# Optimization experiments

Measured on AMD Instinct MI355X. Metric: run time of the kernel, lower is better.

Reference implementation:

```python
import jax, jax.numpy as jnp
import numpy as np

B, T, V, K = 4, 1024, 32000, 50000
EPS_T, EPS_M = 1e-8, 1e-12


def setup_inputs() -> dict:
    key = jax.random.key(0)
    k1, k2, k3, k4 = jax.random.split(key, 4)
    probs = jax.random.uniform(k1, (B, T, V), dtype=jnp.float32)
    # normalize so rows are valid distributions (faithful to softmax outputs)
    probs = probs / probs.sum(-1, keepdims=True)
    target_probs = jax.random.uniform(k2, (K,), dtype=jnp.float32) * (1.0 / K)
    target_oov = jax.random.uniform(k3, (1,), dtype=jnp.float32)
    mask = jnp.ones((B, T), dtype=bool)
    pairs = jax.random.randint(k4, (K, 2), 0, V, dtype=jnp.int64 if jax.config.jax_enable_x64 else jnp.int32)
    return {"probs": probs, "target_probs": target_probs, "target_oov": target_oov,
            "mask": mask, "pairs": pairs}


def reference(probs, target_probs, target_oov, mask, pairs):
    a = pairs[:, 0]  # (K,)
    b = pairs[:, 1]
    p_t = probs[:, :-1, :]   # (B, T-1, V)
    p_t1 = probs[:, 1:, :]
    pair_mask = (mask[:, :-1] & mask[:, 1:]).astype(jnp.float32)  # (B, T-1)
    # gather bigram probs: (B, T-1, K) joint, masked sum over batch/seq
    joint = p_t[..., a] * p_t1[..., b]
    topk_sum = jnp.einsum('btk,bt->k', joint, pair_mask)  # (K,)
    n_pairs = pair_mask.sum()

    # finalize
    n = jnp.maximum(n_pairs, 1.0)
    model_top = jnp.maximum(topk_sum / n, EPS_M)
    model_oov = jnp.clip(1.0 - model_top.sum(), EPS_M, 1.0 - EPS_T)
    tgt = jnp.maximum(target_probs, EPS_T)
    t_oov = jnp.maximum(target_oov[0], EPS_T)
    kl_top = (model_top * (jnp.log(model_top) - jnp.log(tgt))).sum()
    kl_oov = model_oov * (jnp.log(model_oov) - jnp.log(t_oov))
    return kl_top + kl_oov
```

## Files before the change

kernel.cpp:

```cpp
#include <hip/hip_runtime.h>
#include <stdint.h>

#define B_   4
#define T_   1024
#define V_   32000
#define K_   50000
#define N_   (B_*(T_-1))
#define TPB  1024
#define U_   49
#define KP   (TPB*U_)
#define POS_PER_BLK 16
#define G1   ((N_ + POS_PER_BLK - 1)/POS_PER_BLK)
#define EPSTGT 1e-8f
#define EPSMOD 1e-12f
#define W4   (V_/4)
#define NGRP (KP/64)
#define SCAP (2*NGRP)
#define PINV 0xFFFFFFFFu

__device__ __forceinline__ uint32_t bf16rne(float x) {
    uint32_t u = __float_as_uint(x);
    u += 0x7FFFu + ((u >> 16) & 1u);
    return u >> 16;
}
__device__ __forceinline__ uint2 pack4(float4 v) {
    uint2 pk;
    pk.x = bf16rne(v.x) | (bf16rne(v.y) << 16);
    pk.y = bf16rne(v.z) | (bf16rne(v.w) << 16);
    return pk;
}
__device__ __forceinline__ void stage_row(const float* __restrict__ probs, int r,
                                          ushort* dst, int tid) {
    const float4* src = (const float4*)(probs + (size_t)r * V_);
    for (int i = tid; i < W4; i += TPB) {
        *(uint2*)(dst + i * 4) = pack4(src[i]);
    }
}

#define GATHER(pkv, accv) do {                                          \
    uint32_t ao_ = (pkv) >> 16, bo_ = (pkv) & 0xFFFFu;                  \
    ushort av_ = *(const ushort*)(rp + ao_);                            \
    ushort bv_ = *(const ushort*)(rq + bo_);                            \
    accv = fmaf(__uint_as_float((uint32_t)av_ << 16),                   \
                __uint_as_float((uint32_t)bv_ << 16), accv);            \
} while (0)

__global__ __launch_bounds__(1024) void k_perm(const int* __restrict__ pairs,
                                               uint32_t* __restrict__ ppk,
                                               uint32_t* __restrict__ perm,
                                               uint32_t* __restrict__ ovf,
                                               uint32_t* __restrict__ holes) {
    __shared__ uint32_t hist[32][32];
    __shared__ uint32_t boff[32][32];
    __shared__ uint32_t cnt[32][32];
    __shared__ uint32_t binc[32], rot[32];
    __shared__ uint32_t novf, nhole;
    const int tid = threadIdx.x;

    ((uint32_t*)hist)[tid] = 0;
    if (tid == 0) { novf = 0; nhole = 0; }
    __syncthreads();

    for (int k = tid; k < K_; k += 1024) {
        uint32_t a = (uint32_t)pairs[2 * k];
        uint32_t b = (uint32_t)pairs[2 * k + 1];
        atomicAdd(&hist[(a >> 1) & 31][(b >> 1) & 31], 1u);
    }
    __syncthreads();

    if (tid < 32) {
        uint32_t s = 0;
        for (int j = 0; j < 32; ++j) { boff[tid][j] = s; s += hist[tid][j]; }
        binc[tid] = s;
        rot[tid] = ((uint32_t)tid * s) >> 5;
    }
    __syncthreads();
    ((uint32_t*)cnt)[tid] = 0;
    for (int s = tid; s < KP; s += 1024) { ppk[s] = 0; perm[s] = PINV; }
    __syncthreads();

    for (int k = tid; k < K_; k += 1024) {
        uint32_t a = (uint32_t)pairs[2 * k];
        uint32_t b = (uint32_t)pairs[2 * k + 1];
        uint32_t aw = (a >> 1) & 31, bw = (b >> 1) & 31;
        uint32_t j = boff[aw][bw] + atomicAdd(&cnt[aw][bw], 1u);
        uint32_t c = binc[aw];
        uint32_t jp = j + rot[aw]; if (jp >= c) jp -= c;
        uint32_t pk = ((a * 2u) << 16) | (b * 2u);
        if (jp < SCAP) {
            uint32_t s = ((jp >> 1) << 6) + aw + ((jp & 1u) << 5);
            ppk[s] = pk; perm[s] = (uint32_t)k;
        } else {
            uint32_t i = atomicAdd(&novf, 1u);
            ovf[2 * i] = pk; ovf[2 * i + 1] = (uint32_t)k;
        }
    }
    __syncthreads();

    for (int s = tid; s < KP; s += 1024) {
        if (perm[s] == PINV) { uint32_t i = atomicAdd(&nhole, 1u); holes[i] = (uint32_t)s; }
    }
    __syncthreads();
    for (uint32_t i = tid; i < novf; i += 1024) {
        uint32_t s = holes[i];
        ppk[s] = ovf[2 * i]; perm[s] = ovf[2 * i + 1];
    }
}

__global__ void k_mask(const unsigned char* __restrict__ mask, float* __restrict__ scalars) {
    __shared__ int red[16];
    int tid = threadIdx.x;
    int cnt = 0;
    for (int n = tid; n < N_; n += 1024) {
        int b = n / (T_ - 1);
        int t = n - b * (T_ - 1);
        int r = b * T_ + t;
        cnt += (mask[r] && mask[r + 1]) ? 1 : 0;
    }
    for (int off = 32; off > 0; off >>= 1) cnt += __shfl_down(cnt, off, 64);
    int wid = tid >> 6, lid = tid & 63;
    if (lid == 0) red[wid] = cnt;
    __syncthreads();
    if (tid == 0) {
        int s = 0;
        for (int w = 0; w < 16; ++w) s += red[w];
        scalars[0] = (float)s;
    }
}

__global__ __launch_bounds__(TPB) void k_main(
    const float* __restrict__ probs,
    const unsigned char* __restrict__ mask,
    const uint32_t* __restrict__ ppk,
    float* __restrict__ partials, int S, int direct)
{
    __shared__ __align__(16) ushort rows[2][V_];
    __shared__ unsigned char mask_s[32];
    const int tid = threadIdx.x;
    const int g = blockIdx.x;
    const int n0 = g * POS_PER_BLK;
    const int n1 = min(N_, n0 + POS_PER_BLK);

    int r0 = n0 + n0 / (T_ - 1);
    int r1 = r0 + 1;
    const int rbase = r0;
    {
        int rlast = (n1 - 1) + (n1 - 1) / (T_ - 1) + 1;
        int nrows = rlast - rbase + 1;
        if (tid < nrows) mask_s[tid] = mask[rbase + tid];
    }

    float acc[U_];
#pragma unroll
    for (int u = 0; u < U_; ++u) acc[u] = 0.f;

    stage_row(probs, r0, rows[r0 & 1], tid);
    stage_row(probs, r1, rows[r1 & 1], tid);

    const uint32_t* pp = ppk + tid;

    for (int n = n0; n < n1; ++n) {
        const int nn = n + 1;
        const bool more = (nn < n1);
        const int nr0 = nn + nn / (T_ - 1);
        const int nr1 = nr0 + 1;
        const int pre_row = more ? ((nr0 == r1) ? nr1 : nr0) : -1;
        const bool extra = more && (nr0 != r1);
        const int ld_row = (pre_row >= 0) ? pre_row : 0;
        const float4* src = (const float4*)(probs + (size_t)ld_row * V_);

        __syncthreads();

        uint32_t pkA[28];
#pragma unroll
        for (int j = 0; j < 28; ++j) pkA[j] = pp[j * TPB];
        __builtin_amdgcn_sched_barrier(0);
        float4 L0[4];
#pragma unroll
        for (int j = 0; j < 4; ++j) L0[j] = src[tid + j * TPB];
        __builtin_amdgcn_sched_barrier(0);

        const bool active = mask_s[r0 - rbase] && mask_s[r1 - rbase];
        const char* rp = (const char*)rows[r0 & 1];
        const char* rq = (const char*)rows[r1 & 1];

        if (active) {
#pragma unroll
            for (int j = 0; j < 14; ++j) GATHER(pkA[j], acc[j]);
        }
        uint32_t pkB[21];
#pragma unroll
        for (int j = 0; j < 21; ++j) pkB[j] = pp[(28 + j) * TPB];
        __builtin_amdgcn_sched_barrier(0);
        if (active) {
#pragma unroll
            for (int j = 14; j < 28; ++j) GATHER(pkA[j], acc[j]);
        }
        uint2 P0[4];
#pragma unroll
        for (int j = 0; j < 4; ++j) P0[j] = pack4(L0[j]);
        float4 L1[4];
#pragma unroll
        for (int j = 0; j < 4; ++j) {
            int i = tid + (4 + j) * TPB;
            L1[j] = src[(i < W4) ? i : 0];
        }
        __builtin_amdgcn_sched_barrier(0);
        if (active) {
#pragma unroll
            for (int j = 0; j < 21; ++j) GATHER(pkB[j], acc[28 + j]);
        }

        __syncthreads();

        if (pre_row >= 0) {
            ushort* dst = rows[pre_row & 1];
#pragma unroll
            for (int j = 0; j < 4; ++j)
                *(uint2*)(dst + (tid + j * TPB) * 4) = P0[j];
#pragma unroll
            for (int j = 0; j < 4; ++j) {
                int i = tid + (4 + j) * TPB;
                if (i < W4) *(uint2*)(dst + i * 4) = pack4(L1[j]);
            }
            if (extra) stage_row(probs, nr1, rows[nr1 & 1], tid);
        }
        r0 = nr0; r1 = nr1;
    }

    if (direct) {
        float* slot = partials + (size_t)g * KP;
#pragma unroll
        for (int u = 0; u < U_; ++u) slot[u * TPB + tid] = acc[u];
    } else {
        float* slot = partials + (size_t)(g % S) * KP;
#pragma unroll
        for (int u = 0; u < U_; ++u) atomicAdd(slot + u * TPB + tid, acc[u]);
    }
}

__global__ void k_reduce(const float* __restrict__ partials, const uint32_t* __restrict__ perm,
                         const float* __restrict__ tgt,
                         float* __restrict__ scalars, int S) {
    int si = blockIdx.x * 256 + threadIdx.x;
    float n = fmaxf(scalars[0], 1.0f);
    float mt = 0.f, term = 0.f;
    if (si < KP) {
        uint32_t k = perm[si];
        if (k != PINV) {
            float ts = 0.f;
            for (int s = 0; s < S; ++s) ts += partials[(size_t)s * KP + si];
            mt = fmaxf(ts / n, EPSMOD);
            float tg = fmaxf(tgt[k], EPSTGT);
            term = mt * (__logf(mt) - __logf(tg));
        }
    }
    for (int off = 32; off > 0; off >>= 1) {
        mt += __shfl_down(mt, off, 64);
        term += __shfl_down(term, off, 64);
    }
    __shared__ float rm[4], rt[4];
    int wid = threadIdx.x >> 6, lid = threadIdx.x & 63;
    if (lid == 0) { rm[wid] = mt; rt[wid] = term; }
    __syncthreads();
    if (threadIdx.x == 0) {
        float sm = 0.f, st = 0.f;
        for (int w = 0; w < 4; ++w) { sm += rm[w]; st += rt[w]; }
        atomicAdd(&scalars[1], sm);
        atomicAdd(&scalars[2], st);
    }
}

__global__ void k_final(const float* __restrict__ scalars, const float* __restrict__ toov,
                        float* __restrict__ out) {
    float S1 = scalars[1], S2 = scalars[2];
    float moov = 1.f - S1;
    moov = fminf(fmaxf(moov, EPSMOD), 1.f - EPSTGT);
    float tv = fmaxf(toov[0], EPSTGT);
    out[0] = S2 + moov * (__logf(moov) - __logf(tv));
}

extern "C" void kernel_launch(void* const* d_in, const int* in_sizes, int n_in,
                              void* d_out, int out_size, void* d_ws, size_t ws_size,
                              hipStream_t stream) {
    const float* probs = (const float*)d_in[0];
    const float* tgt   = (const float*)d_in[1];
    const float* toov  = (const float*)d_in[2];
    const unsigned char* mask = (const unsigned char*)d_in[3];
    const int* pairs   = (const int*)d_in[4];
    float* out = (float*)d_out;

    char* ws = (char*)d_ws;
    uint32_t* ppk   = (uint32_t*)(ws + 0);
    uint32_t* perm  = (uint32_t*)(ws + 200704);
    uint32_t* ovf   = (uint32_t*)(ws + 401408);
    uint32_t* holes = (uint32_t*)(ws + 801536);
    size_t off_sc = 1002240;
    float* scalars = (float*)(ws + off_sc);
    size_t off_pt = off_sc + 256;
    float* partials = (float*)(ws + off_pt);

    long avail = (long)ws_size - (long)off_pt;
    int smax = (int)(avail / ((long)KP * 4));
    int direct = (smax >= G1) ? 1 : 0;
    int S = direct ? G1 : (smax < 1 ? 1 : (smax > 64 ? 64 : smax));

    hipMemsetAsync(ws + off_sc, 0, 256, stream);
    if (!direct) hipMemsetAsync(partials, 0, (size_t)S * KP * 4, stream);
    k_perm<<<1, 1024, 0, stream>>>(pairs, ppk, perm, ovf, holes);
    k_mask<<<1, 1024, 0, stream>>>(mask, scalars);
    k_main<<<G1, TPB, 0, stream>>>(probs, mask, ppk, partials, S, direct);
    k_reduce<<<(KP + 255) / 256, 256, 0, stream>>>(partials, perm, tgt, scalars, S);
    k_final<<<1, 1, 0, stream>>>(scalars, toov, out);
}
```

Before: 877.1 us.

## Split single-block pair permutation into multi-block histogram/scatter/holes/fill kernels

Replaces the single-workgroup k_perm preprocessing with a pipeline of kernels: a 64-block global-atomic histogram, a one-block prefix sum fused with the mask count, a 64-block scatter, a 64-block hole search and a fill pass. The goal is to spread the pair-permutation setup across many CUs instead of serialising it on one. In exchange it adds kernel launches and global atomics. The order of slots written by the scatter and hole passes is now nondeterministic across blocks.

```diff
diff --git a/kernel.cpp b/kernel.cpp
--- a/kernel.cpp
+++ b/kernel.cpp
@@ -17,6 +17,7 @@
 #define NGRP (KP/64)
 #define SCAP (2*NGRP)
 #define PINV 0xFFFFFFFFu
+#define NBLK_P 64
 
 __device__ __forceinline__ uint32_t bf16rne(float x) {
     uint32_t u = __float_as_uint(x);
@@ -45,71 +46,33 @@
                 __uint_as_float((uint32_t)bv_ << 16), accv);            \
 } while (0)
 
-__global__ __launch_bounds__(1024) void k_perm(const int* __restrict__ pairs,
+
+__global__ __launch_bounds__(1024) void k_hist(const int* __restrict__ pairs,
+                                               uint32_t* __restrict__ hist,
                                                uint32_t* __restrict__ ppk,
-                                               uint32_t* __restrict__ perm,
-                                               uint32_t* __restrict__ ovf,
-                                               uint32_t* __restrict__ holes) {
-    __shared__ uint32_t hist[32][32];
-    __shared__ uint32_t boff[32][32];
-    __shared__ uint32_t cnt[32][32];
-    __shared__ uint32_t binc[32], rot[32];
-    __shared__ uint32_t novf, nhole;
-    const int tid = threadIdx.x;
-
-    ((uint32_t*)hist)[tid] = 0;
-    if (tid == 0) { novf = 0; nhole = 0; }
-    __syncthreads();
-
-    for (int k = tid; k < K_; k += 1024) {
+                                               uint32_t* __restrict__ perm) {
+    int tid = blockIdx.x * 1024 + threadIdx.x;
+    for (int s = tid; s < KP; s += NBLK_P * 1024) { ppk[s] = 0; perm[s] = PINV; }
+    for (int k = tid; k < K_; k += NBLK_P * 1024) {
         uint32_t a = (uint32_t)pairs[2 * k];
         uint32_t b = (uint32_t)pairs[2 * k + 1];
-        atomicAdd(&hist[(a >> 1) & 31][(b >> 1) & 31], 1u);
-    }
-    __syncthreads();
-
+        atomicAdd(&hist[(((a >> 1) & 31) << 5) + ((b >> 1) & 31)], 1u);
+    }
+}
+
+__global__ __launch_bounds__(1024) void k_prefmask(const uint32_t* __restrict__ hist,
+                                                   uint32_t* __restrict__ boff,
+                                                   uint32_t* __restrict__ meta,
+                                                   const unsigned char* __restrict__ mask,
+                                                   float* __restrict__ scalars) {
+    int tid = threadIdx.x;
     if (tid < 32) {
         uint32_t s = 0;
-        for (int j = 0; j < 32; ++j) { boff[tid][j] = s; s += hist[tid][j]; }
-        binc[tid] = s;
-        rot[tid] = ((uint32_t)tid * s) >> 5;
-    }
-    __syncthreads();
-    ((uint32_t*)cnt)[tid] = 0;
-    for (int s = tid; s < KP; s += 1024) { ppk[s] = 0; perm[s] = PINV; }
-    __syncthreads();
-
-    for (int k = tid; k < K_; k += 1024) {
-        uint32_t a = (uint32_t)pairs[2 * k];
-        uint32_t b = (uint32_t)pairs[2 * k + 1];
-        uint32_t aw = (a >> 1) & 31, bw = (b >> 1) & 31;
-        uint32_t j = boff[aw][bw] + atomicAdd(&cnt[aw][bw], 1u);
-        uint32_t c = binc[aw];
-        uint32_t jp = j + rot[aw]; if (jp >= c) jp -= c;
-        uint32_t pk = ((a * 2u) << 16) | (b * 2u);
-        if (jp < SCAP) {
-            uint32_t s = ((jp >> 1) << 6) + aw + ((jp & 1u) << 5);
-            ppk[s] = pk; perm[s] = (uint32_t)k;
-        } else {
-            uint32_t i = atomicAdd(&novf, 1u);
-            ovf[2 * i] = pk; ovf[2 * i + 1] = (uint32_t)k;
-        }
-    }
-    __syncthreads();
-
-    for (int s = tid; s < KP; s += 1024) {
-        if (perm[s] == PINV) { uint32_t i = atomicAdd(&nhole, 1u); holes[i] = (uint32_t)s; }
-    }
-    __syncthreads();
-    for (uint32_t i = tid; i < novf; i += 1024) {
-        uint32_t s = holes[i];
-        ppk[s] = ovf[2 * i]; perm[s] = ovf[2 * i + 1];
-    }
-}
-
-__global__ void k_mask(const unsigned char* __restrict__ mask, float* __restrict__ scalars) {
+        for (int j = 0; j < 32; ++j) { boff[(tid << 5) + j] = s; s += hist[(tid << 5) + j]; }
+        meta[tid] = s;
+        meta[32 + tid] = ((uint32_t)tid * s) >> 5;
+    }
     __shared__ int red[16];
-    int tid = threadIdx.x;
     int cnt = 0;
     for (int n = tid; n < N_; n += 1024) {
         int b = n / (T_ - 1);
@@ -125,6 +88,53 @@
         int s = 0;
         for (int w = 0; w < 16; ++w) s += red[w];
         scalars[0] = (float)s;
+    }
+}
+
+__global__ __launch_bounds__(1024) void k_scatter(const int* __restrict__ pairs,
+                                                  const uint32_t* __restrict__ boff,
+                                                  uint32_t* __restrict__ cnt,
+                                                  uint32_t* __restrict__ meta,
+                                                  uint32_t* __restrict__ ppk,
+                                                  uint32_t* __restrict__ perm,
+                                                  uint32_t* __restrict__ ovf) {
+    int tid = blockIdx.x * 1024 + threadIdx.x;
+    for (int k = tid; k < K_; k += NBLK_P * 1024) {
+        uint32_t a = (uint32_t)pairs[2 * k];
+        uint32_t b = (uint32_t)pairs[2 * k + 1];
+        uint32_t aw = (a >> 1) & 31, bw = (b >> 1) & 31;
+        uint32_t j = boff[(aw << 5) + bw] + atomicAdd(&cnt[(aw << 5) + bw], 1u);
+        uint32_t c = meta[aw];
+        uint32_t jp = j + meta[32 + aw]; if (jp >= c) jp -= c;
+        uint32_t pk = ((a * 2u) << 16) | (b * 2u);
+        if (jp < SCAP) {
+            uint32_t s = ((jp >> 1) << 6) + aw + ((jp & 1u) << 5);
+            ppk[s] = pk; perm[s] = (uint32_t)k;
+        } else {
+            uint32_t i = atomicAdd(&meta[64], 1u);
+            ovf[2 * i] = pk; ovf[2 * i + 1] = (uint32_t)k;
+        }
+    }
+}
+
+__global__ __launch_bounds__(1024) void k_holes(const uint32_t* __restrict__ perm,
+                                                uint32_t* __restrict__ meta,
+                                                uint32_t* __restrict__ holes) {
+    int tid = blockIdx.x * 1024 + threadIdx.x;
+    for (int s = tid; s < KP; s += NBLK_P * 1024) {
+        if (perm[s] == PINV) { uint32_t i = atomicAdd(&meta[65], 1u); holes[i] = (uint32_t)s; }
+    }
+}
+
+__global__ __launch_bounds__(1024) void k_fill(const uint32_t* __restrict__ holes,
+                                               const uint32_t* __restrict__ ovf,
+                                               const uint32_t* __restrict__ meta,
+                                               uint32_t* __restrict__ ppk,
+                                               uint32_t* __restrict__ perm) {
+    uint32_t nv = meta[64];
+    for (uint32_t i = threadIdx.x; i < nv; i += 1024) {
+        uint32_t s = holes[i];
+        ppk[s] = ovf[2 * i]; perm[s] = ovf[2 * i + 1];
     }
 }
 
@@ -295,9 +305,13 @@
     uint32_t* perm  = (uint32_t*)(ws + 200704);
     uint32_t* ovf   = (uint32_t*)(ws + 401408);
     uint32_t* holes = (uint32_t*)(ws + 801536);
-    size_t off_sc = 1002240;
+    uint32_t* hist  = (uint32_t*)(ws + 1002240);
+    uint32_t* boff  = (uint32_t*)(ws + 1006336);
+    uint32_t* cnt   = (uint32_t*)(ws + 1010432);
+    uint32_t* meta  = (uint32_t*)(ws + 1014528);
+    size_t off_sc = 1015040;
     float* scalars = (float*)(ws + off_sc);
-    size_t off_pt = off_sc + 256;
+    size_t off_pt = 1015296;
     float* partials = (float*)(ws + off_pt);
 
     long avail = (long)ws_size - (long)off_pt;
@@ -305,11 +319,15 @@
     int direct = (smax >= G1) ? 1 : 0;
     int S = direct ? G1 : (smax < 1 ? 1 : (smax > 64 ? 64 : smax));
 
-    hipMemsetAsync(ws + off_sc, 0, 256, stream);
+    hipMemsetAsync(ws + 1002240, 0, off_pt - 1002240, stream);
     if (!direct) hipMemsetAsync(partials, 0, (size_t)S * KP * 4, stream);
-    k_perm<<<1, 1024, 0, stream>>>(pairs, ppk, perm, ovf, holes);
-    k_mask<<<1, 1024, 0, stream>>>(mask, scalars);
-    k_main<<<G1, TPB, 0, stream>>>(probs, mask, ppk, partials, S, direct);
-    k_reduce<<<(KP + 255) / 256, 256, 0, stream>>>(partials, perm, tgt, scalars, S);
-    k_final<<<1, 1, 0, stream>>>(scalars, toov, out);
-}
+
+    k_hist    <<<NBLK_P, 1024, 0, stream>>>(pairs, hist, ppk, perm);
+    k_prefmask<<<1, 1024, 0, stream>>>(hist, boff, meta, mask, scalars);
+    k_scatter <<<NBLK_P, 1024, 0, stream>>>(pairs, boff, cnt, meta, ppk, perm, ovf);
+    k_holes   <<<NBLK_P, 1024, 0, stream>>>(perm, meta, holes);
+    k_fill    <<<1, 1024, 0, stream>>>(holes, ovf, meta, ppk, perm);
+    k_main    <<<G1, TPB, 0, stream>>>(probs, mask, ppk, partials, S, direct);
+    k_reduce  <<<(KP + 255) / 256, 256, 0, stream>>>(partials, perm, tgt, scalars, S);
+    k_final   <<<1, 1, 0, stream>>>(scalars, toov, out);
+}
```

Result: faster. 793.0 us (-9.6%).
